# Optimization experiments

Hardware: AMD Instinct MI355X
Metric: run time of the kernel (lower is better)

Reference implementation:

```python
import jax, jax.numpy as jnp
import numpy as np

B, N, C, H = 4, 1024, 768, 12
HD = C // H

def setup_inputs() -> dict:
    key = jax.random.key(0)
    ks = jax.random.split(key, 6)
    s = 0.02
    return {
        "x": jax.random.normal(ks[0], (B, N, C), jnp.float32),
        "attn_bias": jax.random.normal(ks[1], (H, N, N), jnp.float32),
        "qkv_w": jax.random.normal(ks[2], (C, 3 * C), jnp.float32) * s,
        "qkv_b": jax.random.normal(ks[3], (3 * C,), jnp.float32) * s,
        "proj_w": jax.random.normal(ks[4], (C, C), jnp.float32) * s,
        "proj_b": jax.random.normal(ks[5], (C,), jnp.float32) * s,
    }

def reference(x, attn_bias, qkv_w, qkv_b, proj_w, proj_b):
    b, n, c = x.shape
    scale = HD ** -0.5
    qkv = x @ qkv_w + qkv_b                      # [B,N,3C]
    qkv = qkv.reshape(b, n, 3, H, HD)
    q = qkv[:, :, 0].transpose(0, 2, 1, 3)       # [B,H,N,HD]
    k = qkv[:, :, 1].transpose(0, 2, 1, 3)
    v = qkv[:, :, 2].transpose(0, 2, 1, 3)
    attn = jnp.einsum('bhqd,bhkd->bhqk', q, k) * scale
    attn = attn + attn_bias[None]                # broadcast over batch
    attn = jax.nn.softmax(attn, axis=-1)
    y = jnp.einsum('bhqk,bhkd->bhqd', attn, v)   # [B,H,N,HD]
    y = y.transpose(0, 2, 1, 3).reshape(b, n, c)
    return y @ proj_w + proj_b
```

## Files before the change

kernel.cpp:

```cpp
#include <hip/hip_runtime.h>
#include <hip/hip_bf16.h>

constexpr int BATCH = 4;
constexpr int NSEQ  = 1024;
constexpr int CDIM  = 768;
constexpr int NHEAD = 12;
constexpr int HDIM  = 64;
constexpr int MTOT  = BATCH * NSEQ;
constexpr int QKVN  = 3 * CDIM;

typedef __bf16 bf16x8 __attribute__((ext_vector_type(8)));
typedef float  f32x4  __attribute__((ext_vector_type(4)));

__device__ __forceinline__ unsigned short f2bf(float f) {
    unsigned u = __builtin_bit_cast(unsigned, f);
    unsigned r = u + 0x7FFFu + ((u >> 16) & 1u);
    return (unsigned short)(r >> 16);
}

#define GLOAD_LDS16(gp, lp)                                                    \
    __builtin_amdgcn_global_load_lds(                                          \
        (const __attribute__((address_space(1))) void*)(gp),                   \
        (__attribute__((address_space(3))) void*)(lp), 16, 0, 0)

constexpr int NB_X  = MTOT * CDIM / 4 / 256;
constexpr int NB_QW = (QKVN / 32) * (CDIM / 32);
constexpr int NB_PW = (CDIM / 32) * (CDIM / 32);

__device__ __forceinline__ void tcvt_tile(
    const float* __restrict__ in, unsigned short* __restrict__ out,
    int R, int C, int c0, int r0, int tid)
{
    __shared__ unsigned short t[32][33];
    const int tc = tid & 31, tr = tid >> 5;
    #pragma unroll
    for (int i = 0; i < 4; i++)
        t[tc][tr + 8 * i] = f2bf(in[(size_t)(r0 + tr + 8 * i) * C + c0 + tc]);
    __syncthreads();
    #pragma unroll
    for (int i = 0; i < 4; i++)
        out[(size_t)(c0 + tr + 8 * i) * R + r0 + tc] = t[tr + 8 * i][tc];
}

__global__ __launch_bounds__(256) void prep_kernel(
    const float* __restrict__ x,      unsigned short* __restrict__ xb,
    const float* __restrict__ qkv_w,  unsigned short* __restrict__ qwt,
    const float* __restrict__ proj_w, unsigned short* __restrict__ pwt)
{
    const int bid = blockIdx.x;
    const int tid = threadIdx.x;
    if (bid < NB_X) {
        int i = bid * 256 + tid;
        float4 a = reinterpret_cast<const float4*>(x)[i];
        ushort4 h;
        h.x = f2bf(a.x); h.y = f2bf(a.y); h.z = f2bf(a.z); h.w = f2bf(a.w);
        reinterpret_cast<ushort4*>(xb)[i] = h;
    } else if (bid < NB_X + NB_QW) {
        int t = bid - NB_X;
        tcvt_tile(qkv_w, qwt, CDIM, QKVN, (t % (QKVN / 32)) * 32,
                  (t / (QKVN / 32)) * 32, tid);
    } else {
        int t = bid - NB_X - NB_QW;
        tcvt_tile(proj_w, pwt, CDIM, CDIM, (t % (CDIM / 32)) * 32,
                  (t / (CDIM / 32)) * 32, tid);
    }
}

__global__ __launch_bounds__(256) void qkv_gemm(
    const unsigned short* __restrict__ xb,
    const unsigned short* __restrict__ wt,
    const float* __restrict__ bias,
    unsigned short* __restrict__ qbuf, unsigned short* __restrict__ kbuf,
    unsigned short* __restrict__ vtbuf)
{
    __shared__ unsigned short A0[64 * 32], A1[64 * 32];
    __shared__ unsigned short B0[128 * 32], B1[128 * 32];
    const int tid  = threadIdx.x;
    const int lane = tid & 63;
    const int wid  = tid >> 6;
    const int wr = (wid >> 1) * 32, wc = (wid & 1) * 64;
    const int g = lane >> 4, li = lane & 15;
    const int m0 = blockIdx.y * 64;
    const int n0 = blockIdx.x * 128;
    const int srow = lane >> 2;
    const int scol = ((lane & 3) ^ ((lane >> 3) & 3)) * 8;
    const int rsl  = (g ^ ((li >> 1) & 3)) * 8;

#define QSTAGE(K0, AD, BD)                                                     \
    {                                                                          \
        GLOAD_LDS16(&xb[(size_t)(m0 + wid * 16 + srow) * CDIM + (K0) + scol],  \
                    (AD) + wid * 16 * 32);                                     \
        _Pragma("unroll") for (int c = 0; c < 2; c++)                          \
            GLOAD_LDS16(&wt[(size_t)(n0 + wid * 32 + c * 16 + srow) * CDIM + (K0) + scol], \
                        (BD) + (wid * 32 + c * 16) * 32);                      \
    }

#define QCOMPUTE(AS, BS)                                                       \
    {                                                                          \
        bf16x8 a[2], b[4];                                                     \
        _Pragma("unroll") for (int mt = 0; mt < 2; mt++)                       \
            a[mt] = *reinterpret_cast<const bf16x8*>(                          \
                (AS) + (wr + 16 * mt + li) * 32 + rsl);                        \
        _Pragma("unroll") for (int nt = 0; nt < 4; nt++)                       \
            b[nt] = *reinterpret_cast<const bf16x8*>(                          \
                (BS) + (wc + 16 * nt + li) * 32 + rsl);                        \
        _Pragma("unroll") for (int mt = 0; mt < 2; mt++)                       \
            _Pragma("unroll") for (int nt = 0; nt < 4; nt++)                   \
                acc[mt][nt] = __builtin_amdgcn_mfma_f32_16x16x32_bf16(         \
                    a[mt], b[nt], acc[mt][nt], 0, 0, 0);                       \
    }

    f32x4 acc[2][4];
    #pragma unroll
    for (int i = 0; i < 2; i++)
        #pragma unroll
        for (int j = 0; j < 4; j++) acc[i][j] = f32x4{0.f, 0.f, 0.f, 0.f};

    QSTAGE(0, A0, B0);
    __syncthreads();

    for (int j = 0; j < 12; ++j) {
        const int k0 = j * 64;
        QSTAGE(k0 + 32, A1, B1);
        QCOMPUTE(A0, B0);
        __syncthreads();
        if (j < 11) QSTAGE(k0 + 64, A0, B0);
        QCOMPUTE(A1, B1);
        __syncthreads();
    }

    #pragma unroll
    for (int mt = 0; mt < 2; mt++) {
        #pragma unroll
        for (int nt = 0; nt < 4; nt++) {
            int col  = n0 + wc + 16 * nt + li;
            int tsel = col / CDIM;
            int rem  = col - tsel * CDIM;
            int h_ = rem >> 6, d = rem & 63;
            float bv = bias[col];
            float sc = (tsel == 0) ? 0.125f : 1.0f;
            #pragma unroll
            for (int r = 0; r < 4; r++) {
                int m  = m0 + wr + 16 * mt + 4 * g + r;
                int b_ = m >> 10, s = m & 1023;
                unsigned short hv = f2bf((acc[mt][nt][r] + bv) * sc);
                if (tsel == 0)
                    qbuf[(((size_t)b_ * NHEAD + h_) * NSEQ + s) * HDIM + d] = hv;
                else if (tsel == 1)
                    kbuf[(((size_t)b_ * NHEAD + h_) * NSEQ + s) * HDIM + d] = hv;
                else
                    vtbuf[(((size_t)b_ * NHEAD + h_) * HDIM + d) * NSEQ + s] = hv;
            }
        }
    }
#undef QSTAGE
#undef QCOMPUTE
}

__global__ __launch_bounds__(256, 3) void attn_kernel(
    const unsigned short* __restrict__ qbuf,
    const unsigned short* __restrict__ kbuf,
    const unsigned short* __restrict__ vtbuf,
    const float* __restrict__ bias,
    unsigned short* __restrict__ ybuf)
{
    __shared__ unsigned short Kl[2][64 * 64];
    __shared__ unsigned short Vl[2][64 * 64];
    __shared__ unsigned short Ps[4][16][72];

    const int tid  = threadIdx.x;
    const int lane = tid & 63;
    const int wid  = tid >> 6;
    const int g = lane >> 4, li = lane & 15;
    const int srow8 = lane >> 3;
    const int scs   = (lane & 7) ^ srow8;
    const int bh = blockIdx.y;
    const int b_ = bh / NHEAD, h_ = bh % NHEAD;
    const int qw = blockIdx.x * 64 + wid * 16;

    const unsigned short* qb = qbuf + (size_t)bh * NSEQ * HDIM;
    const unsigned short* kb = kbuf + (size_t)bh * NSEQ * HDIM;
    const unsigned short* vb = vtbuf + (size_t)bh * HDIM * NSEQ;
    const float* bb = bias + (size_t)h_ * NSEQ * NSEQ;

#define STAGE_KV(T, KL, VL)                                                    \
    {                                                                          \
        _Pragma("unroll") for (int i = 0; i < 2; i++) {                        \
            GLOAD_LDS16(kb + (size_t)((T) * 64 + wid * 16 + i * 8 + srow8) * HDIM + scs * 8, \
                        (KL) + (wid * 16 + i * 8) * 64);                       \
            GLOAD_LDS16(vb + (size_t)(wid * 16 + i * 8 + srow8) * NSEQ + (T) * 64 + scs * 8, \
                        (VL) + (wid * 16 + i * 8) * 64);                       \
        }                                                                      \
    }

#define COMPUTE_TILE(KS, VS, T)                                                \
    {                                                                          \
        float bv[4][4];                                                        \
        _Pragma("unroll") for (int kt = 0; kt < 4; kt++)                       \
            _Pragma("unroll") for (int r = 0; r < 4; r++)                      \
                bv[kt][r] = bb[(size_t)(qw + 4 * g + r) * NSEQ + (T) * 64 + 16 * kt + li]; \
        f32x4 sacc[4];                                                         \
        _Pragma("unroll") for (int kt = 0; kt < 4; kt++)                       \
            sacc[kt] = f32x4{0.f, 0.f, 0.f, 0.f};                              \
        _Pragma("unroll") for (int kt = 0; kt < 4; kt++)                       \
            _Pragma("unroll") for (int dd = 0; dd < 2; dd++) {                 \
                bf16x8 kf = *reinterpret_cast<const bf16x8*>(                  \
                    (KS) + (16 * kt + li) * 64 + (((4 * dd + g) ^ (li & 7)) * 8)); \
                sacc[kt] = __builtin_amdgcn_mfma_f32_16x16x32_bf16(qf[dd], kf, sacc[kt], 0, 0, 0); \
            }                                                                  \
        _Pragma("unroll") for (int kt = 0; kt < 4; kt++)                       \
            _Pragma("unroll") for (int r = 0; r < 4; r++) {                    \
                float pv = __expf(sacc[kt][r] + bv[kt][r]);                    \
                lpart[r] += pv;                                                \
                Ps[wid][4 * g + r][16 * kt + li] = f2bf(pv);                   \
            }                                                                  \
        _Pragma("unroll") for (int kk = 0; kk < 2; kk++) {                     \
            bf16x8 pf = *reinterpret_cast<const bf16x8*>(&Ps[wid][li][32 * kk + 8 * g]); \
            _Pragma("unroll") for (int dt = 0; dt < 4; dt++) {                 \
                bf16x8 vf = *reinterpret_cast<const bf16x8*>(                  \
                    (VS) + (16 * dt + li) * 64 + (((4 * kk + g) ^ (li & 7)) * 8)); \
                oacc[dt] = __builtin_amdgcn_mfma_f32_16x16x32_bf16(pf, vf, oacc[dt], 0, 0, 0); \
            }                                                                  \
        }                                                                      \
    }

    bf16x8 qf[2];
    #pragma unroll
    for (int dd = 0; dd < 2; dd++)
        qf[dd] = *reinterpret_cast<const bf16x8*>(&qb[(size_t)(qw + li) * HDIM + 32 * dd + 8 * g]);

    f32x4 oacc[4];
    #pragma unroll
    for (int dt = 0; dt < 4; dt++) oacc[dt] = f32x4{0.f, 0.f, 0.f, 0.f};
    float lpart[4] = {0.f, 0.f, 0.f, 0.f};

    STAGE_KV(0, Kl[0], Vl[0]);
    __syncthreads();

    for (int j = 0; j < 8; ++j) {
        const int tA = 2 * j;
        STAGE_KV(tA + 1, Kl[1], Vl[1]);
        COMPUTE_TILE(Kl[0], Vl[0], tA);
        __syncthreads();

        if (j < 7) STAGE_KV(tA + 2, Kl[0], Vl[0]);
        COMPUTE_TILE(Kl[1], Vl[1], tA + 1);
        __syncthreads();
    }

    float linv[4];
    #pragma unroll
    for (int r = 0; r < 4; r++) {
        float s = lpart[r];
        s += __shfl_xor(s, 1);
        s += __shfl_xor(s, 2);
        s += __shfl_xor(s, 4);
        s += __shfl_xor(s, 8);
        linv[r] = 1.f / s;
    }
    #pragma unroll
    for (int dt = 0; dt < 4; dt++)
        #pragma unroll
        for (int r = 0; r < 4; r++) {
            float o = oacc[dt][r] * linv[r];
            int sq = qw + 4 * g + r;
            ybuf[((size_t)b_ * NSEQ + sq) * CDIM + h_ * HDIM + 16 * dt + li] = f2bf(o);
        }
#undef STAGE_KV
#undef COMPUTE_TILE
}

__global__ __launch_bounds__(256) void proj_gemm(
    const unsigned short* __restrict__ yb,
    const unsigned short* __restrict__ pwt,
    const float* __restrict__ bias, float* __restrict__ out)
{
    __shared__ unsigned short A0[64 * 32], A1[64 * 32];
    __shared__ unsigned short B0[128 * 32], B1[128 * 32];
    const int tid  = threadIdx.x;
    const int lane = tid & 63;
    const int wid  = tid >> 6;
    const int wr = (wid >> 1) * 32, wc = (wid & 1) * 64;
    const int g = lane >> 4, li = lane & 15;
    const int m0 = blockIdx.y * 64;
    const int n0 = blockIdx.x * 128;
    const int srow = lane >> 2;
    const int scol = ((lane & 3) ^ ((lane >> 3) & 3)) * 8;
    const int rsl  = (g ^ ((li >> 1) & 3)) * 8;

#define PSTAGE(K0, AD, BD)                                                     \
    {                                                                          \
        GLOAD_LDS16(&yb[(size_t)(m0 + wid * 16 + srow) * CDIM + (K0) + scol],  \
                    (AD) + wid * 16 * 32);                                     \
        _Pragma("unroll") for (int c = 0; c < 2; c++)                          \
            GLOAD_LDS16(&pwt[(size_t)(n0 + wid * 32 + c * 16 + srow) * CDIM + (K0) + scol], \
                        (BD) + (wid * 32 + c * 16) * 32);                      \
    }

#define PCOMPUTE(AS, BS)                                                       \
    {                                                                          \
        bf16x8 a[2], b[4];                                                     \
        _Pragma("unroll") for (int mt = 0; mt < 2; mt++)                       \
            a[mt] = *reinterpret_cast<const bf16x8*>(                          \
                (AS) + (wr + 16 * mt + li) * 32 + rsl);                        \
        _Pragma("unroll") for (int nt = 0; nt < 4; nt++)                       \
            b[nt] = *reinterpret_cast<const bf16x8*>(                          \
                (BS) + (wc + 16 * nt + li) * 32 + rsl);                        \
        _Pragma("unroll") for (int mt = 0; mt < 2; mt++)                       \
            _Pragma("unroll") for (int nt = 0; nt < 4; nt++)                   \
                acc[mt][nt] = __builtin_amdgcn_mfma_f32_16x16x32_bf16(         \
                    a[mt], b[nt], acc[mt][nt], 0, 0, 0);                       \
    }

    f32x4 acc[2][4];
    #pragma unroll
    for (int i = 0; i < 2; i++)
        #pragma unroll
        for (int j = 0; j < 4; j++) acc[i][j] = f32x4{0.f, 0.f, 0.f, 0.f};

    PSTAGE(0, A0, B0);
    __syncthreads();

    for (int j = 0; j < 12; ++j) {
        const int k0 = j * 64;
        PSTAGE(k0 + 32, A1, B1);
        PCOMPUTE(A0, B0);
        __syncthreads();
        if (j < 11) PSTAGE(k0 + 64, A0, B0);
        PCOMPUTE(A1, B1);
        __syncthreads();
    }

    #pragma unroll
    for (int mt = 0; mt < 2; mt++)
        #pragma unroll
        for (int nt = 0; nt < 4; nt++) {
            int col = n0 + wc + 16 * nt + li;
            float bv = bias[col];
            #pragma unroll
            for (int r = 0; r < 4; r++) {
                int m = m0 + wr + 16 * mt + 4 * g + r;
                out[(size_t)m * CDIM + col] = acc[mt][nt][r] + bv;
            }
        }
#undef PSTAGE
#undef PCOMPUTE
}

extern "C" void kernel_launch(void* const* d_in, const int* in_sizes, int n_in,
                              void* d_out, int out_size, void* d_ws, size_t ws_size,
                              hipStream_t stream) {
    const float* x         = (const float*)d_in[0];
    const float* attn_bias = (const float*)d_in[1];
    const float* qkv_w     = (const float*)d_in[2];
    const float* qkv_b     = (const float*)d_in[3];
    const float* proj_w    = (const float*)d_in[4];
    const float* proj_b    = (const float*)d_in[5];
    float* out = (float*)d_out;

    const size_t per = (size_t)BATCH * NHEAD * NSEQ * HDIM;
    unsigned short* qbuf  = (unsigned short*)d_ws;
    unsigned short* kbuf  = qbuf + per;
    unsigned short* vtbuf = kbuf + per;
    unsigned short* xb    = vtbuf + per;
    unsigned short* qwt   = xb + per;
    unsigned short* pwt   = qwt + (size_t)QKVN * CDIM;
    unsigned short* ybuf  = xb;

    prep_kernel<<<NB_X + NB_QW + NB_PW, 256, 0, stream>>>(
        x, xb, qkv_w, qwt, proj_w, pwt);

    qkv_gemm<<<dim3(QKVN / 128, MTOT / 64), 256, 0, stream>>>(
        xb, qwt, qkv_b, qbuf, kbuf, vtbuf);
    attn_kernel<<<dim3(NSEQ / 64, BATCH * NHEAD), 256, 0, stream>>>(
        qbuf, kbuf, vtbuf, attn_bias, ybuf);
    proj_gemm<<<dim3(CDIM / 128, MTOT / 64), 256, 0, stream>>>(
        ybuf, pwt, proj_b, out);
}
```

Before: 100.8 us.

## Triple-buffer QKV GEMM LDS stages with partial vmcnt waits

The QKV projection GEMM moves from double to triple buffering of its A/B shared-memory tiles. Each step now waits only until the oldest stage's global-to-LDS loads have landed (vmcnt(3)) instead of draining everything at __syncthreads, so two stages of loads stay in flight during compute. This adds about 12KB of LDS per block, which may lower occupancy, and relies on a hand-written waitcnt/barrier sequence being correct.

```diff
diff --git a/kernel.cpp b/kernel.cpp
--- a/kernel.cpp
+++ b/kernel.cpp
@@ -73,8 +73,8 @@
     unsigned short* __restrict__ qbuf, unsigned short* __restrict__ kbuf,
     unsigned short* __restrict__ vtbuf)
 {
-    __shared__ unsigned short A0[64 * 32], A1[64 * 32];
-    __shared__ unsigned short B0[128 * 32], B1[128 * 32];
+    __shared__ unsigned short A0[64 * 32], A1[64 * 32], A2[64 * 32];
+    __shared__ unsigned short B0[128 * 32], B1[128 * 32], B2[128 * 32];
     const int tid  = threadIdx.x;
     const int lane = tid & 63;
     const int wid  = tid >> 6;
@@ -110,6 +110,21 @@
                     a[mt], b[nt], acc[mt][nt], 0, 0, 0);                       \
     }
 
+#define WAITBAR3()                                                             \
+    {                                                                          \
+        asm volatile("s_waitcnt vmcnt(3)" ::: "memory");                       \
+        __builtin_amdgcn_sched_barrier(0);                                     \
+        __builtin_amdgcn_s_barrier();                                          \
+        __builtin_amdgcn_sched_barrier(0);                                     \
+    }
+#define WAITBAR0()                                                             \
+    {                                                                          \
+        asm volatile("s_waitcnt vmcnt(0)" ::: "memory");                       \
+        __builtin_amdgcn_sched_barrier(0);                                     \
+        __builtin_amdgcn_s_barrier();                                          \
+        __builtin_amdgcn_sched_barrier(0);                                     \
+    }
+
     f32x4 acc[2][4];
     #pragma unroll
     for (int i = 0; i < 2; i++)
@@ -117,16 +132,26 @@
         for (int j = 0; j < 4; j++) acc[i][j] = f32x4{0.f, 0.f, 0.f, 0.f};
 
     QSTAGE(0, A0, B0);
-    __syncthreads();
-
-    for (int j = 0; j < 12; ++j) {
-        const int k0 = j * 64;
-        QSTAGE(k0 + 32, A1, B1);
+    QSTAGE(32, A1, B1);
+    WAITBAR3();
+
+    for (int j = 0; j < 8; ++j) {
+        const int k0 = j * 96;
+        QSTAGE(k0 + 64, A2, B2);
         QCOMPUTE(A0, B0);
-        __syncthreads();
-        if (j < 11) QSTAGE(k0 + 64, A0, B0);
-        QCOMPUTE(A1, B1);
-        __syncthreads();
+        WAITBAR3();
+        if (j < 7) {
+            QSTAGE(k0 + 96, A0, B0);
+            QCOMPUTE(A1, B1);
+            WAITBAR3();
+            QSTAGE(k0 + 128, A1, B1);
+            QCOMPUTE(A2, B2);
+            WAITBAR3();
+        } else {
+            QCOMPUTE(A1, B1);
+            WAITBAR0();
+            QCOMPUTE(A2, B2);
+        }
     }
 
     #pragma unroll
@@ -155,6 +180,8 @@
     }
 #undef QSTAGE
 #undef QCOMPUTE
+#undef WAITBAR3
+#undef WAITBAR0
 }
 
 __global__ __launch_bounds__(256, 3) void attn_kernel(
```

Result: no change. 99.01 us (-1.8%).
